# Kernel tuning notes

Measured on AMD Instinct MI355X. Metric: run time of the kernel, lower is better.

Reference implementation:

```python
import jax, jax.numpy as jnp
import numpy as np

N = 1024
D = 256            # model_dims
H = D // 2         # hidden_dim = 128
L = 3              # num_levels
EPS = 1e-5


def ln(x, g, b):
    mu = jnp.mean(x, axis=-1, keepdims=True)
    v = jnp.mean((x - mu) ** 2, axis=-1, keepdims=True)
    return (x - mu) / jnp.sqrt(v + EPS) * g + b


def setup_inputs() -> dict:
    key = jax.random.key(0)
    ks = jax.random.split(key, 24)
    s = 0.02
    inp = {
        'atomic_numbers': jax.random.randint(ks[0], (N,), 0, 100),
        'positions': jax.random.normal(ks[1], (N, 3), dtype=jnp.float32) * 3.0,
        'emb': jax.random.normal(ks[2], (100, H), dtype=jnp.float32) * s,
        # distance_expansion: Linear(3, H) + SiLU + LayerNorm(H)
        'de_W': jax.random.normal(ks[3], (L, H), dtype=jnp.float32) * s,
        'de_b': jnp.zeros((H,), jnp.float32),
        'de_g': jnp.ones((H,), jnp.float32),
        'de_be': jnp.zeros((H,), jnp.float32),
        'msg_W': jax.random.normal(ks[4], (L, 2 * H, H), dtype=jnp.float32) * s,
        'msg_b': jnp.zeros((L, H), jnp.float32),
        'msg_g': jnp.ones((L, H), jnp.float32),
        'msg_be': jnp.zeros((L, H), jnp.float32),
        'upd_W': jax.random.normal(ks[5], (L, 2 * H, H), dtype=jnp.float32) * s,
        'upd_b': jnp.zeros((L, H), jnp.float32),
        'upd_g': jnp.ones((L, H), jnp.float32),
        'upd_be': jnp.zeros((L, H), jnp.float32),
        # final proj: Linear(3H, D) + LayerNorm(D)
        'fp_W': jax.random.normal(ks[6], (L * H, D), dtype=jnp.float32) * s,
        'fp_b': jnp.zeros((D,), jnp.float32),
        'fp_g': jnp.ones((D,), jnp.float32),
        'fp_be': jnp.zeros((D,), jnp.float32),
    }
    return inp


def reference(atomic_numbers, positions, emb, de_W, de_b, de_g, de_be,
              msg_W, msg_b, msg_g, msg_be, upd_W, upd_b, upd_g, upd_be,
              fp_W, fp_b, fp_g, fp_be):
    x = emb[atomic_numbers]                                    # [N,H]
    diff = positions[:, None, :] - positions[None, :, :]       # [N,N,3]
    sq = jnp.sum(diff * diff, axis=-1)
    d = jnp.where(sq > 0, jnp.sqrt(jnp.where(sq > 0, sq, 1.0)), 0.0)  # safe norm
    scales = jnp.stack([jnp.exp(-d), jnp.exp(-d / 2), jnp.exp(-d / 4)], axis=-1)  # [N,N,3]
    ew = ln(jax.nn.silu(scales @ de_W + de_b), de_g, de_be)    # [N,N,H]

    level_feats = []
    for lvl in range(L):
        Wi, Wj = msg_W[lvl, :H], msg_W[lvl, H:]
        # cat([x_i, x_j]) @ W == x_i @ Wi + x_j @ Wj
        pre = x @ Wi                                           # [N,H]
        prj = x @ Wj                                           # [N,H]
        m = ln(jax.nn.silu(pre[:, None, :] + prj[None, :, :] + msg_b[lvl]),
               msg_g[lvl], msg_be[lvl])                        # [N,N,H]
        msum = jnp.einsum('ijh,ijh->ih', m, ew)                # sum over j
        u = jnp.concatenate([x, msum], axis=-1)                # [N,2H]
        x = x + ln(jax.nn.silu(u @ upd_W[lvl] + upd_b[lvl]), upd_g[lvl], upd_be[lvl])
        level_feats.append(jnp.mean(x, axis=0))

    combined = jnp.concatenate(level_feats, axis=0)            # [3H]
    return ln(combined @ fp_W + fp_b, fp_g, fp_be)             # [D]
```

## Files before the change

kernel.cpp:

```cpp
#include <hip/hip_runtime.h>
#include <math.h>

constexpr int N_ = 1024;
constexpr int H_ = 128;
constexpr int D_ = 256;
constexpr int L_ = 3;
constexpr float EPS_ = 1e-5f;
constexpr float LOG2E_ = 1.44269504f;
constexpr int KLUT_ = 8192;
constexpr float DMAX_ = 40.0f;
constexpr float TSCALE_ = (KLUT_ - 1) / DMAX_;
constexpr float TMAX_ = (float)(KLUT_ - 1) - 0.001f;

__device__ __forceinline__ float fsig(float v) {
    float e = __builtin_amdgcn_exp2f(v * -LOG2E_);
    return __builtin_amdgcn_rcpf(1.0f + e);
}

template <int CTRL>
__device__ __forceinline__ float rowadd(float x) {
    int y = __builtin_amdgcn_update_dpp(0, __float_as_int(x), CTRL, 0xF, 0xF, true);
    return x + __int_as_float(y);
}
__device__ __forceinline__ float rowreduce16(float x) {
    x = rowadd<0x128>(x);
    x = rowadd<0x124>(x);
    x = rowadd<0x122>(x);
    x = rowadd<0x121>(x);
    return x;
}

#define LD8(dst, src)                                                     \
    {                                                                     \
        float4 t0_ = *(const float4*)(src);                               \
        float4 t1_ = *(const float4*)((src) + 4);                         \
        dst[0] = t0_.x; dst[1] = t0_.y; dst[2] = t0_.z; dst[3] = t0_.w;   \
        dst[4] = t1_.x; dst[5] = t1_.y; dst[6] = t1_.z; dst[7] = t1_.w;   \
    }

__global__ void k_lut(const float* __restrict__ deW, const float* __restrict__ deb,
                      const float* __restrict__ deg, const float* __restrict__ debe,
                      float* __restrict__ lut) {
    int e = blockIdx.x * 4 + (threadIdx.x >> 6);
    int lane = threadIdx.x & 63;
    float d = e * (DMAX_ / (KLUT_ - 1));
    float s0 = expf(-d), s1 = expf(-0.5f * d), s2 = expf(-0.25f * d);
    float v[2];
    float sum = 0.f, ssq = 0.f;
#pragma unroll
    for (int kk = 0; kk < 2; ++kk) {
        int c = lane + 64 * kk;
        float a = s0 * deW[c] + s1 * deW[H_ + c] + s2 * deW[2 * H_ + c] + deb[c];
        float sg = 1.f / (1.f + expf(-a));
        v[kk] = a * sg;
        sum += v[kk]; ssq += v[kk] * v[kk];
    }
#pragma unroll
    for (int mask = 1; mask < 64; mask <<= 1) {
        sum += __shfl_xor(sum, mask);
        ssq += __shfl_xor(ssq, mask);
    }
    float mu = sum * (1.f / H_);
    float var = ssq * (1.f / H_) - mu * mu;
    float rstd = 1.f / sqrtf(var + EPS_);
#pragma unroll
    for (int kk = 0; kk < 2; ++kk) {
        int c = lane + 64 * kk;
        lut[e * H_ + c] = (v[kk] - mu) * rstd * deg[c] + debe[c];
    }
}

__global__ void k_embed_gemm(const int* __restrict__ an, const float* __restrict__ emb,
                             const float* __restrict__ W, const float* __restrict__ b,
                             float* __restrict__ x, float* __restrict__ preb,
                             float* __restrict__ prj) {
    int i = blockIdx.x;
    int t = threadIdx.x;
    __shared__ float xr[H_];
    if (t < H_) {
        float xv = emb[an[i] * H_ + t];
        xr[t] = xv;
        x[i * H_ + t] = xv;
    }
    __syncthreads();
    int h = t & (H_ - 1);
    int off = (t >= H_) ? H_ : 0;
    float s = 0.f;
#pragma unroll 4
    for (int k = 0; k < H_; k += 4) {
        float4 xv = *(const float4*)&xr[k];
        s = fmaf(xv.x, W[(off + k) * H_ + h], s);
        s = fmaf(xv.y, W[(off + k + 1) * H_ + h], s);
        s = fmaf(xv.z, W[(off + k + 2) * H_ + h], s);
        s = fmaf(xv.w, W[(off + k + 3) * H_ + h], s);
    }
    if (t >= H_) prj[i * H_ + h] = s;
    else         preb[i * H_ + h] = s + b[h];
}

__device__ __forceinline__ void prf_step(int JT, int p, int cb, const int* jinfo,
                                         const float* __restrict__ lut,
                                         const float* __restrict__ prjR,
                                         float (&EW)[8], float (&TM)[8]) {
    int jw = (JT & (N_ - 1)) + p;
    int jof = jinfo[jw];
    const float* lp = (const float*)((const char*)lut + jof) + cb;
    LD8(EW, lp);
    LD8(TM, prjR + jw * H_ + cb);
}

__device__ __forceinline__ void cmp_step(const float (&EW)[8], float (&TM)[8],
                                         const float (&pbv)[8],
                                         float (&acc1)[8], float (&acc2)[8]) {
    float sum = 0.f, ssq = 0.f;
#pragma unroll
    for (int k = 0; k < 8; ++k) {
        float w = pbv[k] + TM[k];
        float vv = w * fsig(w);
        TM[k] = vv; sum += vv; ssq = fmaf(vv, vv, ssq);
    }
    sum = rowreduce16(sum);
    ssq = rowreduce16(ssq);
    float mu = sum * (1.f / H_);
    float var = fmaf(ssq, 1.f / H_, -mu * mu);
    float rstd = __builtin_amdgcn_rsqf(var + EPS_);
    float c1 = -mu * rstd;
#pragma unroll
    for (int k = 0; k < 8; ++k) {
        float t = fmaf(TM[k], rstd, c1);
        acc1[k] = fmaf(t, EW[k], acc1[k]);
        acc2[k] += EW[k];
    }
}

__global__ __launch_bounds__(512, 4) void k_pair(
    const float* __restrict__ pos, const float* __restrict__ x,
    const float* __restrict__ prebR, const float* __restrict__ prjR,
    const float* __restrict__ lut,
    const float* __restrict__ mgp, const float* __restrict__ mbep,
    const float* __restrict__ uW, const float* __restrict__ ub,
    const float* __restrict__ ug, const float* __restrict__ ube,
    const float* __restrict__ Wn, const float* __restrict__ bn,
    float* __restrict__ xout, float* __restrict__ lmean,
    float* __restrict__ prebW, float* __restrict__ prjW) {
    const int i = blockIdx.x;
    const int tid = threadIdx.x;
    const int w = tid >> 6;
    const int lane = tid & 63;
    const int g = lane >> 4;
    const int q = lane & 15;
    const int p = w * 4 + g;
    const int cb = q * 8;

    __shared__ int jinfo[N_];
    __shared__ float red[32][H_];
    __shared__ float msums[H_], xrow[H_], xs[H_];
    __shared__ float part[4][H_];
    __shared__ float r4[2][2];

    float pbv[8], acc1[8], acc2[8];
    LD8(pbv, prebR + i * H_ + cb);
#pragma unroll
    for (int k = 0; k < 8; ++k) { acc1[k] = 0.f; acc2[k] = 0.f; }

    const float pix = pos[3 * i], piy = pos[3 * i + 1], piz = pos[3 * i + 2];
    for (int j = tid; j < N_; j += 512) {
        float dx = pix - pos[3 * j];
        float dy = piy - pos[3 * j + 1];
        float dz = piz - pos[3 * j + 2];
        float sq = fmaf(dx, dx, fmaf(dy, dy, dz * dz));
        float d = __builtin_amdgcn_sqrtf(sq);
        float tf = fminf(d * TSCALE_, TMAX_);
        int i0 = (int)(tf + 0.5f);
        jinfo[j] = i0 * (H_ * 4);
    }
    if (tid < H_) xrow[tid] = x[i * H_ + tid];
    __syncthreads();

    float ewA[8], tmA[8], ewB[8], tmB[8];
    prf_step(0, p, cb, jinfo, lut, prjR, ewA, tmA);
    __builtin_amdgcn_sched_barrier(0);
    for (int jt = 0; jt < N_; jt += 64) {
        prf_step(jt + 32, p, cb, jinfo, lut, prjR, ewB, tmB);
        __builtin_amdgcn_sched_barrier(0);
        cmp_step(ewA, tmA, pbv, acc1, acc2);
        __builtin_amdgcn_sched_barrier(0);
        prf_step(jt + 64, p, cb, jinfo, lut, prjR, ewA, tmA);
        __builtin_amdgcn_sched_barrier(0);
        cmp_step(ewB, tmB, pbv, acc1, acc2);
        __builtin_amdgcn_sched_barrier(0);
    }

    float mgv[8], mbev[8], acc[8];
    LD8(mgv, mgp + cb);
    LD8(mbev, mbep + cb);
#pragma unroll
    for (int k = 0; k < 8; ++k)
        acc[k] = mgv[k] * acc1[k] + mbev[k] * acc2[k];
    *(float4*)&red[p][cb] = make_float4(acc[0], acc[1], acc[2], acc[3]);
    *(float4*)&red[p][cb + 4] = make_float4(acc[4], acc[5], acc[6], acc[7]);
    __syncthreads();
    if (tid < H_) {
        float s = 0.f;
#pragma unroll
        for (int pp = 0; pp < 32; ++pp) s += red[pp][tid];
        msums[tid] = s;
    }
    __syncthreads();

    int h = tid & (H_ - 1);
    int seg = tid >> 7;
    const float* src = (seg == 0) ? xrow : (seg == 1) ? xrow + 64
                     : (seg == 2) ? msums : msums + 64;
    const float* Wp = uW + (seg * 64) * H_ + h;
    float s2 = 0.f;
#pragma unroll 4
    for (int k = 0; k < 64; k += 4) {
        float4 uv = *(const float4*)&src[k];
        s2 = fmaf(uv.x, Wp[(k + 0) * H_], s2);
        s2 = fmaf(uv.y, Wp[(k + 1) * H_], s2);
        s2 = fmaf(uv.z, Wp[(k + 2) * H_], s2);
        s2 = fmaf(uv.w, Wp[(k + 3) * H_], s2);
    }
    part[seg][h] = s2;
    __syncthreads();
    float v = 0.f;
    if (tid < H_) {
        float sv = part[0][tid] + part[1][tid] + part[2][tid] + part[3][tid] + ub[tid];
        v = sv * fsig(sv);
    }
    float sum = v, ssq = v * v;
#pragma unroll
    for (int mask = 1; mask < 64; mask <<= 1) {
        sum += __shfl_xor(sum, mask);
        ssq += __shfl_xor(ssq, mask);
    }
    if (tid < H_ && (tid & 63) == 0) { r4[tid >> 6][0] = sum; r4[tid >> 6][1] = ssq; }
    __syncthreads();
    if (tid < H_) {
        sum = r4[0][0] + r4[1][0];
        ssq = r4[0][1] + r4[1][1];
        float mu = sum * (1.f / H_);
        float var = fmaf(ssq, 1.f / H_, -mu * mu);
        float rstd = rsqrtf(var + EPS_);
        float xn = xrow[tid] + fmaf((v - mu) * rstd, ug[tid], ube[tid]);
        xs[tid] = xn;
        xout[i * H_ + tid] = xn;
        atomicAdd(&lmean[tid], xn);
    }

    if (Wn) {
        __syncthreads();
        int which = tid >> 8;
        int kh = (tid >> 7) & 1;
        const float* Wp2 = Wn + (which * H_ + kh * 64) * H_ + h;
        const float* xsrc = xs + kh * 64;
        float s3 = 0.f;
#pragma unroll 4
        for (int k = 0; k < 64; k += 4) {
            float4 xv = *(const float4*)&xsrc[k];
            s3 = fmaf(xv.x, Wp2[(k + 0) * H_], s3);
            s3 = fmaf(xv.y, Wp2[(k + 1) * H_], s3);
            s3 = fmaf(xv.z, Wp2[(k + 2) * H_], s3);
            s3 = fmaf(xv.w, Wp2[(k + 3) * H_], s3);
        }
        part[(which << 1) | kh][h] = s3;
        __syncthreads();
        if (tid < 256) {
            int wh = tid >> 7, h3 = tid & 127;
            float val = part[wh * 2][h3] + part[wh * 2 + 1][h3];
            if (wh) prjW[i * H_ + h3] = val;
            else    prebW[i * H_ + h3] = val + bn[h3];
        }
    }
}

__global__ void k_final(const float* __restrict__ lmean, const float* __restrict__ fpW,
                        const float* __restrict__ fpb, const float* __restrict__ fpg,
                        const float* __restrict__ fpbe, float* __restrict__ out) {
    int t = threadIdx.x;
    __shared__ float comb[L_ * H_];
    comb[t] = lmean[t] * (1.f / N_);
    if (t < L_ * H_ - D_) comb[D_ + t] = lmean[D_ + t] * (1.f / N_);
    __syncthreads();
    float s = fpb[t];
#pragma unroll 8
    for (int k = 0; k < L_ * H_; ++k)
        s = fmaf(comb[k], fpW[k * D_ + t], s);
    float sum = s, ssq = s * s;
#pragma unroll
    for (int mask = 1; mask < 64; mask <<= 1) {
        sum += __shfl_xor(sum, mask);
        ssq += __shfl_xor(ssq, mask);
    }
    __shared__ float r4[4][2];
    int wv = t >> 6;
    if ((t & 63) == 0) { r4[wv][0] = sum; r4[wv][1] = ssq; }
    __syncthreads();
    sum = r4[0][0] + r4[1][0] + r4[2][0] + r4[3][0];
    ssq = r4[0][1] + r4[1][1] + r4[2][1] + r4[3][1];
    float mu = sum * (1.f / D_);
    float var = fmaf(ssq, 1.f / D_, -mu * mu);
    float rstd = rsqrtf(var + EPS_);
    out[t] = fmaf((s - mu) * rstd, fpg[t], fpbe[t]);
}

extern "C" void kernel_launch(void* const* d_in, const int* in_sizes, int n_in,
                              void* d_out, int out_size, void* d_ws, size_t ws_size,
                              hipStream_t stream) {
    const int*   an    = (const int*)d_in[0];
    const float* pos   = (const float*)d_in[1];
    const float* emb   = (const float*)d_in[2];
    const float* deW   = (const float*)d_in[3];
    const float* deb   = (const float*)d_in[4];
    const float* deg   = (const float*)d_in[5];
    const float* debe  = (const float*)d_in[6];
    const float* msgW  = (const float*)d_in[7];
    const float* msgb  = (const float*)d_in[8];
    const float* msgg  = (const float*)d_in[9];
    const float* msgbe = (const float*)d_in[10];
    const float* updW  = (const float*)d_in[11];
    const float* updb  = (const float*)d_in[12];
    const float* updg  = (const float*)d_in[13];
    const float* updbe = (const float*)d_in[14];
    const float* fpW   = (const float*)d_in[15];
    const float* fpb   = (const float*)d_in[16];
    const float* fpg   = (const float*)d_in[17];
    const float* fpbe  = (const float*)d_in[18];
    float* out = (float*)d_out;

    float* ws    = (float*)d_ws;
    float* x     = ws;
    float* prebA = x + N_ * H_;
    float* prjA  = prebA + N_ * H_;
    float* prebB = prjA + N_ * H_;
    float* prjB  = prebB + N_ * H_;
    float* lmean = prjB + N_ * H_;
    float* lut   = lmean + L_ * H_;

    hipMemsetAsync(lmean, 0, L_ * H_ * sizeof(float), stream);
    k_lut<<<KLUT_ / 4, 256, 0, stream>>>(deW, deb, deg, debe, lut);
    k_embed_gemm<<<N_, 256, 0, stream>>>(an, emb, msgW, msgb, x, prebA, prjA);
    for (int lvl = 0; lvl < L_; ++lvl) {
        const float* pR  = (lvl & 1) ? prebB : prebA;
        const float* prR = (lvl & 1) ? prjB  : prjA;
        float* pW  = (lvl & 1) ? prebA : prebB;
        float* prW = (lvl & 1) ? prjA  : prjB;
        const float* Wn = (lvl < L_ - 1) ? msgW + (lvl + 1) * 2 * H_ * H_ : nullptr;
        const float* bn = (lvl < L_ - 1) ? msgb + (lvl + 1) * H_ : nullptr;
        k_pair<<<N_, 512, 0, stream>>>(pos, x, pR, prR, lut,
                                       msgg + lvl * H_, msgbe + lvl * H_,
                                       updW + lvl * 2 * H_ * H_, updb + lvl * H_,
                                       updg + lvl * H_, updbe + lvl * H_,
                                       Wn, bn, x, lmean + lvl * H_, pW, prW);
    }
    k_final<<<1, D_, 0, stream>>>(lmean, fpW, fpb, fpg, fpbe, out);
}
```

Before: 234.4 us.

## Stage prj rows via global_load_lds double buffers and use packed float2 math

Moves the per-tile prj row fetch from register loads to asynchronous global_load_lds into per-wave double-buffered LDS slices, then reads them back from LDS while the next tile is in flight. Rewrites the pair compute on two-wide float vectors so the compiler can emit packed FP32 ops. The aim is to hide global latency and cut VALU instruction count. No explicit waitcnt or barrier is placed between the async LDS writes and the reads, which risks race hazards. The extra 32KB of LDS may also lower occupancy.

```diff
diff --git a/kernel.cpp b/kernel.cpp
--- a/kernel.cpp
+++ b/kernel.cpp
@@ -5,6 +5,7 @@
 constexpr int H_ = 128;
 constexpr int D_ = 256;
 constexpr int L_ = 3;
+constexpr int NT_ = N_ / 32;
 constexpr float EPS_ = 1e-5f;
 constexpr float LOG2E_ = 1.44269504f;
 constexpr int KLUT_ = 8192;
@@ -12,6 +13,8 @@
 constexpr float TSCALE_ = (KLUT_ - 1) / DMAX_;
 constexpr float TMAX_ = (float)(KLUT_ - 1) - 0.001f;
 
+typedef float v2f __attribute__((ext_vector_type(2)));
+
 __device__ __forceinline__ float fsig(float v) {
     float e = __builtin_amdgcn_exp2f(v * -LOG2E_);
     return __builtin_amdgcn_rcpf(1.0f + e);
@@ -36,6 +39,14 @@
         float4 t1_ = *(const float4*)((src) + 4);                         \
         dst[0] = t0_.x; dst[1] = t0_.y; dst[2] = t0_.z; dst[3] = t0_.w;   \
         dst[4] = t1_.x; dst[5] = t1_.y; dst[6] = t1_.z; dst[7] = t1_.w;   \
+    }
+
+#define LD8V(dst, src)                                                    \
+    {                                                                     \
+        float4 t0_ = *(const float4*)(src);                               \
+        float4 t1_ = *(const float4*)((src) + 4);                         \
+        dst[0] = (v2f){t0_.x, t0_.y}; dst[1] = (v2f){t0_.z, t0_.w};       \
+        dst[2] = (v2f){t1_.x, t1_.y}; dst[3] = (v2f){t1_.z, t1_.w};       \
     }
 
 __global__ void k_lut(const float* __restrict__ deW, const float* __restrict__ deb,
@@ -98,40 +109,61 @@
     else         preb[i * H_ + h] = s + b[h];
 }
 
-__device__ __forceinline__ void prf_step(int JT, int p, int cb, const int* jinfo,
-                                         const float* __restrict__ lut,
-                                         const float* __restrict__ prjR,
-                                         float (&EW)[8], float (&TM)[8]) {
-    int jw = (JT & (N_ - 1)) + p;
-    int jof = jinfo[jw];
-    const float* lp = (const float*)((const char*)lut + jof) + cb;
-    LD8(EW, lp);
-    LD8(TM, prjR + jw * H_ + cb);
-}
-
-__device__ __forceinline__ void cmp_step(const float (&EW)[8], float (&TM)[8],
-                                         const float (&pbv)[8],
-                                         float (&acc1)[8], float (&acc2)[8]) {
-    float sum = 0.f, ssq = 0.f;
-#pragma unroll
-    for (int k = 0; k < 8; ++k) {
-        float w = pbv[k] + TM[k];
-        float vv = w * fsig(w);
-        TM[k] = vv; sum += vv; ssq = fmaf(vv, vv, ssq);
-    }
-    sum = rowreduce16(sum);
-    ssq = rowreduce16(ssq);
+__device__ __forceinline__ void stage(const float* __restrict__ prjR, int jt, int w,
+                                      int lane, float (*buf)[512]) {
+    const float* g0 = prjR + (jt + 4 * w + (lane >> 5)) * H_ + (lane & 31) * 4;
+    __builtin_amdgcn_global_load_lds(
+        (const __attribute__((address_space(1))) void*)g0,
+        (__attribute__((address_space(3))) void*)&buf[w][0], 16, 0, 0);
+    const float* g1 = g0 + 2 * H_;
+    __builtin_amdgcn_global_load_lds(
+        (const __attribute__((address_space(1))) void*)g1,
+        (__attribute__((address_space(3))) void*)&buf[w][256], 16, 0, 0);
+}
+
+__device__ __forceinline__ void cmp_step(const v2f (&EW)[4], const float* rp,
+                                         const v2f (&pbv)[4],
+                                         v2f (&acc1)[4], v2f (&acc2)[4]) {
+    float4 pa = *(const float4*)rp;
+    float4 pb4 = *(const float4*)(rp + 4);
+    v2f tm[4] = {{pa.x, pa.y}, {pa.z, pa.w}, {pb4.x, pb4.y}, {pb4.z, pb4.w}};
+    v2f sum2 = {0.f, 0.f}, ssq2 = {0.f, 0.f};
+#pragma unroll
+    for (int k = 0; k < 4; ++k) {
+        v2f wv = pbv[k] + tm[k];
+        v2f sg;
+        sg.x = fsig(wv.x);
+        sg.y = fsig(wv.y);
+        v2f vv = wv * sg;
+        tm[k] = vv;
+        sum2 += vv;
+        ssq2 += vv * vv;
+    }
+    float sum = rowreduce16(sum2.x + sum2.y);
+    float ssq = rowreduce16(ssq2.x + ssq2.y);
     float mu = sum * (1.f / H_);
     float var = fmaf(ssq, 1.f / H_, -mu * mu);
     float rstd = __builtin_amdgcn_rsqf(var + EPS_);
     float c1 = -mu * rstd;
-#pragma unroll
-    for (int k = 0; k < 8; ++k) {
-        float t = fmaf(TM[k], rstd, c1);
-        acc1[k] = fmaf(t, EW[k], acc1[k]);
+    v2f rstd2 = {rstd, rstd}, c12 = {c1, c1};
+#pragma unroll
+    for (int k = 0; k < 4; ++k) {
+        v2f t = tm[k] * rstd2 + c12;
+        acc1[k] += t * EW[k];
         acc2[k] += EW[k];
     }
 }
+
+#define PAIR_BODY(T, BUFRD, BUFWR, LUTRD, LUTWR)                              \
+    {                                                                         \
+        if ((T) + 1 < NT_) {                                                  \
+            stage(prjR, ((T) + 1) * 32, w, lane, BUFWR);                      \
+            int jof_ = jinfo[((T) + 1) * 32 + p];                             \
+            LD8V(LUTWR, (const float*)((const char*)lut + jof_) + cb);        \
+        }                                                                     \
+        __builtin_amdgcn_sched_barrier(0);                                    \
+        cmp_step(LUTRD, &BUFRD[w][g * 128 + q * 8], pbv, acc1, acc2);         \
+    }
 
 __global__ __launch_bounds__(512, 4) void k_pair(
     const float* __restrict__ pos, const float* __restrict__ x,
@@ -152,16 +184,18 @@
     const int p = w * 4 + g;
     const int cb = q * 8;
 
+    __shared__ float bufA[8][512];
+    __shared__ float bufB[8][512];
     __shared__ int jinfo[N_];
     __shared__ float red[32][H_];
     __shared__ float msums[H_], xrow[H_], xs[H_];
     __shared__ float part[4][H_];
     __shared__ float r4[2][2];
 
-    float pbv[8], acc1[8], acc2[8];
-    LD8(pbv, prebR + i * H_ + cb);
-#pragma unroll
-    for (int k = 0; k < 8; ++k) { acc1[k] = 0.f; acc2[k] = 0.f; }
+    v2f pbv[4], acc1[4], acc2[4];
+    LD8V(pbv, prebR + i * H_ + cb);
+#pragma unroll
+    for (int k = 0; k < 4; ++k) { acc1[k] = (v2f){0.f, 0.f}; acc2[k] = (v2f){0.f, 0.f}; }
 
     const float pix = pos[3 * i], piy = pos[3 * i + 1], piz = pos[3 * i + 2];
     for (int j = tid; j < N_; j += 512) {
@@ -177,28 +211,25 @@
     if (tid < H_) xrow[tid] = x[i * H_ + tid];
     __syncthreads();
 
-    float ewA[8], tmA[8], ewB[8], tmB[8];
-    prf_step(0, p, cb, jinfo, lut, prjR, ewA, tmA);
-    __builtin_amdgcn_sched_barrier(0);
-    for (int jt = 0; jt < N_; jt += 64) {
-        prf_step(jt + 32, p, cb, jinfo, lut, prjR, ewB, tmB);
-        __builtin_amdgcn_sched_barrier(0);
-        cmp_step(ewA, tmA, pbv, acc1, acc2);
-        __builtin_amdgcn_sched_barrier(0);
-        prf_step(jt + 64, p, cb, jinfo, lut, prjR, ewA, tmA);
-        __builtin_amdgcn_sched_barrier(0);
-        cmp_step(ewB, tmB, pbv, acc1, acc2);
-        __builtin_amdgcn_sched_barrier(0);
-    }
-
-    float mgv[8], mbev[8], acc[8];
-    LD8(mgv, mgp + cb);
-    LD8(mbev, mbep + cb);
-#pragma unroll
-    for (int k = 0; k < 8; ++k)
-        acc[k] = mgv[k] * acc1[k] + mbev[k] * acc2[k];
-    *(float4*)&red[p][cb] = make_float4(acc[0], acc[1], acc[2], acc[3]);
-    *(float4*)&red[p][cb + 4] = make_float4(acc[4], acc[5], acc[6], acc[7]);
+    v2f lutA[4], lutB[4];
+    stage(prjR, 0, w, lane, bufA);
+    {
+        int jof_ = jinfo[p];
+        LD8V(lutA, (const float*)((const char*)lut + jof_) + cb);
+    }
+    for (int t = 0; t < NT_; t += 2) {
+        PAIR_BODY(t, bufA, bufB, lutA, lutB);
+        PAIR_BODY(t + 1, bufB, bufA, lutB, lutA);
+    }
+
+    v2f mgv[4], mbev[4], accv[4];
+    LD8V(mgv, mgp + cb);
+    LD8V(mbev, mbep + cb);
+#pragma unroll
+    for (int k = 0; k < 4; ++k)
+        accv[k] = mgv[k] * acc1[k] + mbev[k] * acc2[k];
+    *(float4*)&red[p][cb] = make_float4(accv[0].x, accv[0].y, accv[1].x, accv[1].y);
+    *(float4*)&red[p][cb + 4] = make_float4(accv[2].x, accv[2].y, accv[3].x, accv[3].y);
     __syncthreads();
     if (tid < H_) {
         float s = 0.f;
```

After: 246.9 us. 1.05x slower.
